# Kernel tuning notes

Measured on AMD Instinct MI355X. Metric: run time of the kernel, lower is better.

## Reference

```python
import jax, jax.numpy as jnp
import numpy as np

BATCH = 32768
NUM_CLASSES = 1000

def setup_inputs() -> dict:
    key = jax.random.key(0)
    k1, k2 = jax.random.split(key)
    input = jax.random.normal(k1, (BATCH, NUM_CLASSES), dtype=jnp.float32)
    target = jax.random.randint(k2, (BATCH, NUM_CLASSES), 0, 2, dtype=jnp.int32)
    return {"input": input, "target": target}

def reference(input, target):
    # LSEP: loss = log(1 + sum_{i} sum_{p in pos_i} sum_{n in neg_i} exp(x[i,n] - x[i,p]))
    # The pair sum factorizes per sample:
    #   sum_{p,n} exp(x_n - x_p) = (sum_{n in neg} exp(x_n)) * (sum_{p in pos} exp(-x_p))
    pos = target > 0
    neg = target == 0
    s_neg = jnp.sum(jnp.where(neg, jnp.exp(input), 0.0), axis=1)   # [B]
    s_pos = jnp.sum(jnp.where(pos, jnp.exp(-input), 0.0), axis=1)  # [B]
    total = jnp.sum(s_neg * s_pos)
    return jnp.log1p(total).reshape(1).astype(jnp.float32)
```

## Files before the change

### kernel.cpp

```cpp
#include <hip/hip_runtime.h>
#include <math.h>

#define BATCH   32768
#define NCLS    1000
#define NC4     250
#define NBLOCKS 2048
#define NWAVES  (NBLOCKS * 4)

__global__ __launch_bounds__(256) void lsep_row_kernel(
    const float* __restrict__ x,
    const int*   __restrict__ t,
    float* __restrict__ wave_out) {

    const int tid   = threadIdx.x;
    const int lane  = tid & 63;
    const int gwave = blockIdx.x * 4 + (tid >> 6);

    float acc = 0.0f;

    #pragma unroll
    for (int r = 0; r < BATCH / NWAVES; ++r) {
        const int row = gwave + r * NWAVES;
        const float4* xr = (const float4*)(x + (size_t)row * NCLS);
        const int4*   tr = (const int4*)(t + (size_t)row * NCLS);

        float4 xv[4];
        int4   tv[4];
        #pragma unroll
        for (int j = 0; j < 4; ++j) {
            const int idx = lane + 64 * j;
            if (idx < NC4) {
                xv[j] = xr[idx];
                tv[j] = tr[idx];
            }
        }

        float sn = 0.0f, sp = 0.0f;
        #pragma unroll
        for (int j = 0; j < 4; ++j) {
            const int idx = lane + 64 * j;
            if (idx < NC4) {
                {   float e = __expf(xv[j].x); float r1 = __builtin_amdgcn_rcpf(e);
                    if (tv[j].x == 0) sn += e; else sp += r1; }
                {   float e = __expf(xv[j].y); float r1 = __builtin_amdgcn_rcpf(e);
                    if (tv[j].y == 0) sn += e; else sp += r1; }
                {   float e = __expf(xv[j].z); float r1 = __builtin_amdgcn_rcpf(e);
                    if (tv[j].z == 0) sn += e; else sp += r1; }
                {   float e = __expf(xv[j].w); float r1 = __builtin_amdgcn_rcpf(e);
                    if (tv[j].w == 0) sn += e; else sp += r1; }
            }
        }

        #pragma unroll
        for (int off = 32; off > 0; off >>= 1) {
            sn += __shfl_down(sn, off, 64);
            sp += __shfl_down(sp, off, 64);
        }

        if (lane == 0) acc += sn * sp;
    }

    if (lane == 0) wave_out[gwave] = acc;
}

__global__ __launch_bounds__(256) void lsep_reduce_kernel(
    const float* __restrict__ wave_out,
    float* __restrict__ out) {

    const int tid = threadIdx.x;
    const float4* r4 = (const float4*)wave_out;

    float4 a[8];
    #pragma unroll
    for (int j = 0; j < 8; ++j)
        a[j] = r4[tid + 256 * j];

    float v = 0.0f;
    #pragma unroll
    for (int j = 0; j < 8; ++j)
        v += (a[j].x + a[j].y) + (a[j].z + a[j].w);

    #pragma unroll
    for (int off = 32; off > 0; off >>= 1)
        v += __shfl_down(v, off, 64);

    __shared__ float sv[4];
    const int wave = tid >> 6;
    const int lane = tid & 63;
    if (lane == 0) sv[wave] = v;
    __syncthreads();

    if (tid == 0) {
        float total = (sv[0] + sv[1]) + (sv[2] + sv[3]);
        out[0] = log1pf(total);
    }
}

extern "C" void kernel_launch(void* const* d_in, const int* in_sizes, int n_in,
                              void* d_out, int out_size, void* d_ws, size_t ws_size,
                              hipStream_t stream) {
    const float* x = (const float*)d_in[0];
    const int*   t = (const int*)d_in[1];
    float* out     = (float*)d_out;
    float* wave_ws = (float*)d_ws;

    lsep_row_kernel<<<NBLOCKS, 256, 0, stream>>>(x, t, wave_ws);
    lsep_reduce_kernel<<<1, 256, 0, stream>>>(wave_ws, out);
}
```

Baseline: 272.4 us.

## Software-pipeline row loads and replace exp+rcp with sign-selected single exp

Each wave now loads the next row's float4/int4 chunks into registers while it computes the current row, so memory latency overlaps the exp work. The per-element math computes a single exp of x or -x chosen by the target, instead of exp plus a reciprocal. Double buffering raises register use, and a memory-bound kernel may gain little from the lighter math.

Result: no change. 271.2 us (-0.4%).

```diff
diff --git a/kernel.cpp b/kernel.cpp
--- a/kernel.cpp
+++ b/kernel.cpp
@@ -6,6 +6,18 @@
 #define NC4     250
 #define NBLOCKS 2048
 #define NWAVES  (NBLOCKS * 4)
+#define RPW     (BATCH / NWAVES)
+
+__device__ __forceinline__ void acc4(float4 xv, int4 tv, float& sn, float& sp) {
+    float e0 = __expf(tv.x == 0 ? xv.x : -xv.x);
+    float e1 = __expf(tv.y == 0 ? xv.y : -xv.y);
+    float e2 = __expf(tv.z == 0 ? xv.z : -xv.z);
+    float e3 = __expf(tv.w == 0 ? xv.w : -xv.w);
+    sn += (tv.x == 0) ? e0 : 0.0f;  sp += (tv.x == 0) ? 0.0f : e0;
+    sn += (tv.y == 0) ? e1 : 0.0f;  sp += (tv.y == 0) ? 0.0f : e1;
+    sn += (tv.z == 0) ? e2 : 0.0f;  sp += (tv.z == 0) ? 0.0f : e2;
+    sn += (tv.w == 0) ? e3 : 0.0f;  sp += (tv.w == 0) ? 0.0f : e3;
+}
 
 __global__ __launch_bounds__(256) void lsep_row_kernel(
     const float* __restrict__ x,
@@ -16,39 +28,49 @@
     const int lane  = tid & 63;
     const int gwave = blockIdx.x * 4 + (tid >> 6);
 
+    const bool tail = (lane + 192 < NC4);
+
+    const float4* xp = (const float4*)x + (size_t)gwave * NC4;
+    const int4*   tp = (const int4*)t + (size_t)gwave * NC4;
+    const size_t rstep = (size_t)NWAVES * NC4;
+
+    float4 xv0, xv1, xv2, xv3;
+    int4   tv0, tv1, tv2, tv3;
+
+    xv0 = xp[lane];       tv0 = tp[lane];
+    xv1 = xp[lane + 64];  tv1 = tp[lane + 64];
+    xv2 = xp[lane + 128]; tv2 = tp[lane + 128];
+    if (tail) { xv3 = xp[lane + 192]; tv3 = tp[lane + 192]; }
+
     float acc = 0.0f;
 
     #pragma unroll
-    for (int r = 0; r < BATCH / NWAVES; ++r) {
-        const int row = gwave + r * NWAVES;
-        const float4* xr = (const float4*)(x + (size_t)row * NCLS);
-        const int4*   tr = (const int4*)(t + (size_t)row * NCLS);
-
-        float4 xv[4];
-        int4   tv[4];
-        #pragma unroll
-        for (int j = 0; j < 4; ++j) {
-            const int idx = lane + 64 * j;
-            if (idx < NC4) {
-                xv[j] = xr[idx];
-                tv[j] = tr[idx];
-            }
-        }
+    for (int r = 0; r < RPW; ++r) {
+        const bool more = (r + 1 < RPW);
+        const float4* xn = xp + (size_t)(r + 1) * rstep;
+        const int4*   tn = tp + (size_t)(r + 1) * rstep;
 
         float sn = 0.0f, sp = 0.0f;
-        #pragma unroll
-        for (int j = 0; j < 4; ++j) {
-            const int idx = lane + 64 * j;
-            if (idx < NC4) {
-                {   float e = __expf(xv[j].x); float r1 = __builtin_amdgcn_rcpf(e);
-                    if (tv[j].x == 0) sn += e; else sp += r1; }
-                {   float e = __expf(xv[j].y); float r1 = __builtin_amdgcn_rcpf(e);
-                    if (tv[j].y == 0) sn += e; else sp += r1; }
-                {   float e = __expf(xv[j].z); float r1 = __builtin_amdgcn_rcpf(e);
-                    if (tv[j].z == 0) sn += e; else sp += r1; }
-                {   float e = __expf(xv[j].w); float r1 = __builtin_amdgcn_rcpf(e);
-                    if (tv[j].w == 0) sn += e; else sp += r1; }
-            }
+
+        {
+            float4 xc = xv0; int4 tc = tv0;
+            if (more) { xv0 = xn[lane]; tv0 = tn[lane]; }
+            acc4(xc, tc, sn, sp);
+        }
+        {
+            float4 xc = xv1; int4 tc = tv1;
+            if (more) { xv1 = xn[lane + 64]; tv1 = tn[lane + 64]; }
+            acc4(xc, tc, sn, sp);
+        }
+        {
+            float4 xc = xv2; int4 tc = tv2;
+            if (more) { xv2 = xn[lane + 128]; tv2 = tn[lane + 128]; }
+            acc4(xc, tc, sn, sp);
+        }
+        if (tail) {
+            float4 xc = xv3; int4 tc = tv3;
+            if (more) { xv3 = xn[lane + 192]; tv3 = tn[lane + 192]; }
+            acc4(xc, tc, sn, sp);
         }
 
         #pragma unroll
```
